# Kernel optimization log

Measured on AMD Instinct MI355X. Metric: run time of the kernel, lower is better.

Reference implementation:

```python
import jax, jax.numpy as jnp
import numpy as np
import math

B, C, T = 4, 512, 2048
H = 8            # num_heads
G = 32           # GroupNorm groups (GroupNorm32 in ADM-style code)
EPS = 1e-5


def setup_inputs() -> dict:
    key = jax.random.key(0)
    ks = jax.random.split(key, 7)
    x = jax.random.normal(ks[0], (B, C, T), jnp.float32)
    norm_scale = 1.0 + 0.02 * jax.random.normal(ks[1], (C,), jnp.float32)
    norm_bias = 0.02 * jax.random.normal(ks[2], (C,), jnp.float32)
    qkv_w = 0.02 * jax.random.normal(ks[3], (3 * C, C), jnp.float32)  # 1x1 conv == matmul
    qkv_b = 0.02 * jax.random.normal(ks[4], (3 * C,), jnp.float32)
    proj_w = 0.02 * jax.random.normal(ks[5], (C, C), jnp.float32)
    proj_b = 0.02 * jax.random.normal(ks[6], (C,), jnp.float32)
    return {"x": x, "norm_scale": norm_scale, "norm_bias": norm_bias,
            "qkv_w": qkv_w, "qkv_b": qkv_b, "proj_w": proj_w, "proj_b": proj_b}


def _group_norm(x, scale, bias):
    # x: [B, C, T]; 32-group norm over (C/G, T) per group
    b, c, t = x.shape
    xg = x.reshape(b, G, (c // G) * t)
    mean = jnp.mean(xg, axis=-1, keepdims=True)
    var = jnp.var(xg, axis=-1, keepdims=True)
    xg = (xg - mean) * jax.lax.rsqrt(var + EPS)
    return xg.reshape(b, c, t) * scale[None, :, None] + bias[None, :, None]


def reference(x, norm_scale, norm_bias, qkv_w, qkv_b, proj_w, proj_b):
    b, c, t = x.shape
    ch = c // H
    h = _group_norm(x, norm_scale, norm_bias)
    qkv = jnp.einsum('oc,bct->bot', qkv_w, h) + qkv_b[None, :, None]  # [B, 3C, T]
    q, k, v = jnp.split(qkv, 3, axis=1)
    q = q.reshape(b * H, ch, t)
    k = k.reshape(b * H, ch, t)
    v = v.reshape(b * H, ch, t)
    scale = 1.0 / math.sqrt(math.sqrt(ch))
    w = jnp.einsum('bct,bcs->bts', q * scale, k * scale)              # [B*H, T, T]
    w = jax.nn.softmax(w.astype(jnp.float32), axis=-1).astype(qkv.dtype)
    a = jnp.einsum('bts,bcs->bct', w, v).reshape(b, c, t)             # [B, C, T]
    out = jnp.einsum('oc,bct->bot', proj_w, a) + proj_b[None, :, None]
    return x + out
```

## Files before the change

kernel.cpp:

```cpp
#include <hip/hip_runtime.h>

typedef short bf16x8 __attribute__((ext_vector_type(8)));
typedef float f32x4 __attribute__((ext_vector_type(4)));
typedef float f32x16 __attribute__((ext_vector_type(16)));
typedef unsigned short u16;
typedef unsigned int u32;

constexpr int B = 4, C = 512, T = 2048, H = 8, G = 32;
constexpr int CH = C / H;
constexpr int CPG = C / G;
constexpr float EPS = 1e-5f;
constexpr float SCLQ = 0.18033688011112042f;

__device__ __forceinline__ u16 f2bf(float f) {
  union { float f; u32 u; } v; v.f = f;
  return (u16)((v.u + 0x7FFFu + ((v.u >> 16) & 1u)) >> 16);
}

__device__ __forceinline__ u32 cvtpk(float lo, float hi) {
  u32 r;
  asm("v_cvt_pk_bf16_f32 %0, %1, %2" : "=v"(r) : "v"(lo), "v"(hi));
  return r;
}

__device__ __forceinline__ void gload16(const void* g, void* lds) {
  __builtin_amdgcn_global_load_lds(
      (const __attribute__((address_space(1))) void*)g,
      (__attribute__((address_space(3))) void*)lds, 16, 0, 0);
}

__device__ __forceinline__ void pl32swap(u32& a, u32& b) {
  asm("v_permlane32_swap_b32 %0, %1" : "+v"(a), "+v"(b));
}

template <int ROWS>
__device__ __forceinline__ void stage_swz_8w(u16* lds, const u16* gsrc, int ldk) {
  const int tid = threadIdx.x;
  const int w = tid >> 6, lane = tid & 63;
#pragma unroll
  for (int i = 0; i < ROWS / 64; ++i) {
    const int chunk = i * 8 + w;
    const int row = chunk * 8 + (lane >> 3);
    const int col = ((lane & 7) * 8) ^ ((row & 7) << 3);
    gload16(gsrc + (size_t)row * ldk + col, (char*)lds + chunk * 1024);
  }
}

__global__ __launch_bounds__(256) void prep_k(const float* __restrict__ x,
                                              float* __restrict__ stats,
                                              const float* __restrict__ s1,
                                              u16* __restrict__ d1, int n1,
                                              const float* __restrict__ s2,
                                              u16* __restrict__ d2, int n2) {
  __shared__ float red[8];
  const int bid = blockIdx.x;
  if (bid >= 128) {
    int i = (bid - 128) * 256 + threadIdx.x;
    const float4* src = (const float4*)s1;
    uint2* dst = (uint2*)d1;
    if (i >= n1) { i -= n1; if (i >= n2) return; src = (const float4*)s2; dst = (uint2*)d2; }
    float4 v = src[i];
    uint2 pk;
    pk.x = cvtpk(v.x, v.y);
    pk.y = cvtpk(v.z, v.w);
    dst[i] = pk;
    return;
  }
  const int bg = bid;
  const float4* xp = (const float4*)(x + (size_t)bg * CPG * T);
  float s = 0.f, ss = 0.f;
  for (int i = threadIdx.x; i < CPG * T / 4; i += 256) {
    float4 v = xp[i];
    s += v.x + v.y + v.z + v.w;
    ss += v.x * v.x + v.y * v.y + v.z * v.z + v.w * v.w;
  }
  for (int off = 32; off; off >>= 1) {
    s += __shfl_down(s, off);
    ss += __shfl_down(ss, off);
  }
  const int w = threadIdx.x >> 6;
  if ((threadIdx.x & 63) == 0) { red[w] = s; red[4 + w] = ss; }
  __syncthreads();
  if (threadIdx.x == 0) {
    float S = red[0] + red[1] + red[2] + red[3];
    float SS = red[4] + red[5] + red[6] + red[7];
    const float inv = 1.f / (float)(CPG * T);
    float mean = S * inv;
    float var = SS * inv - mean * mean;
    stats[bg * 2] = mean;
    stats[bg * 2 + 1] = rsqrtf(var + EPS);
  }
}

__global__ __launch_bounds__(256) void gn_apply_k(const float* __restrict__ x,
                                                  const float* __restrict__ stats,
                                                  const float* __restrict__ gsc,
                                                  const float* __restrict__ gbi,
                                                  u16* __restrict__ ht) {
  const int b = blockIdx.y;
  const int t0 = blockIdx.x * 16;
#pragma unroll
  for (int p = 0; p < 2; ++p) {
    const int c = p * 256 + threadIdx.x;
    const int bg = b * G + (c >> 4);
    const float mean = stats[bg * 2], rstd = stats[bg * 2 + 1];
    const float sc = gsc[c] * rstd;
    const float bi = gbi[c] - mean * sc;
    const float4* xp = (const float4*)(x + ((size_t)b * C + c) * T + t0);
#pragma unroll
    for (int j = 0; j < 4; ++j) {
      float4 v = xp[j];
      const int t = t0 + j * 4;
      u16* hp = ht + ((size_t)b * T + t) * C + c;
      hp[0]     = f2bf(v.x * sc + bi);
      hp[C]     = f2bf(v.y * sc + bi);
      hp[2 * C] = f2bf(v.z * sc + bi);
      hp[3 * C] = f2bf(v.w * sc + bi);
    }
  }
}

__global__ __launch_bounds__(512, 2) void qkv_gemm_k(const u16* __restrict__ ht,
                                                     const u16* __restrict__ wq,
                                                     const float* __restrict__ qkvb,
                                                     u16* __restrict__ qo,
                                                     u16* __restrict__ kvo_k,
                                                     u16* __restrict__ kvo_v) {
  __shared__ u16 As[2][128 * 64];
  __shared__ u16 Bs[2][128 * 64];
  const int bid = blockIdx.x;
  const int wg = (bid & 7) * 96 + (bid >> 3);
  const int nt = wg % 12;
  const int mtb = wg / 12;
  const int mt = mtb & 15, b = mtb >> 4;
  const u16* Ab = ht + ((size_t)b * T + mt * 128) * C;
  const u16* Bb = wq + (size_t)nt * 128 * C;
  const int tid = threadIdx.x, lane = tid & 63, w = tid >> 6;
  const int wr = w >> 1, wc = w & 1, l15 = lane & 15, lhi = lane >> 4;
  const int swz = (l15 & 7) << 3;
  constexpr int NK = C / 64;

  const f32x4 vzero = {0.f, 0.f, 0.f, 0.f};
  f32x4 acc[2][4];
#pragma unroll
  for (int m = 0; m < 2; ++m)
#pragma unroll
    for (int n = 0; n < 4; ++n) acc[m][n] = vzero;

  stage_swz_8w<128>(As[0], Ab, C);
  stage_swz_8w<128>(Bs[0], Bb, C);
  asm volatile("s_waitcnt vmcnt(0)" ::: "memory");
  __builtin_amdgcn_s_barrier();
  asm volatile("" ::: "memory");

  int cur = 0;
  for (int kt = 0; kt < NK; ++kt) {
    if (kt + 1 < NK) {
      stage_swz_8w<128>(As[cur ^ 1], Ab + (kt + 1) * 64, C);
      stage_swz_8w<128>(Bs[cur ^ 1], Bb + (kt + 1) * 64, C);
    }
#pragma unroll
    for (int kk = 0; kk < 2; ++kk) {
      const int koff = (kk * 32 + lhi * 8) ^ swz;
      bf16x8 af[2], bfv[4];
#pragma unroll
      for (int m = 0; m < 2; ++m)
        af[m] = *(const bf16x8*)&As[cur][(wr * 32 + m * 16 + l15) * 64 + koff];
#pragma unroll
      for (int n = 0; n < 4; ++n)
        bfv[n] = *(const bf16x8*)&Bs[cur][(wc * 64 + n * 16 + l15) * 64 + koff];
#pragma unroll
      for (int m = 0; m < 2; ++m)
#pragma unroll
        for (int n = 0; n < 4; ++n)
          acc[m][n] = __builtin_amdgcn_mfma_f32_16x16x32_bf16(af[m], bfv[n], acc[m][n], 0, 0, 0);
    }
    if (kt + 1 < NK) {
      asm volatile("s_waitcnt vmcnt(0)" ::: "memory");
      __builtin_amdgcn_s_barrier();
      asm volatile("" ::: "memory");
    }
    cur ^= 1;
  }
#pragma unroll
  for (int n = 0; n < 4; ++n) {
    const int o = nt * 128 + wc * 64 + n * 16 + l15;
    const float bias = qkvb[o];
    const int which = o >> 9, rem = o & 511, hh = rem >> 6, d = rem & 63;
    const size_t bh = (size_t)b * H + hh;
#pragma unroll
    for (int m = 0; m < 2; ++m) {
      const int tbase = mt * 128 + wr * 32 + m * 16 + lhi * 4;
      float v0 = acc[m][n][0] + bias, v1 = acc[m][n][1] + bias;
      float v2 = acc[m][n][2] + bias, v3 = acc[m][n][3] + bias;
      if (which == 0) { v0 *= SCLQ; v1 *= SCLQ; v2 *= SCLQ; v3 *= SCLQ; }
      const u32 w01 = cvtpk(v0, v1), w23 = cvtpk(v2, v3);
      if (which == 2) {
        uint2 pk; pk.x = w01; pk.y = w23;
        *(uint2*)&kvo_v[(bh * CH + d) * T + tbase] = pk;
      } else {
        u16* dst = (which == 0) ? qo : kvo_k;
        dst[(bh * T + tbase) * CH + d]     = (u16)(w01 & 0xffff);
        dst[(bh * T + tbase + 1) * CH + d] = (u16)(w01 >> 16);
        dst[(bh * T + tbase + 2) * CH + d] = (u16)(w23 & 0xffff);
        dst[(bh * T + tbase + 3) * CH + d] = (u16)(w23 >> 16);
      }
    }
  }
}

__global__ __launch_bounds__(512, 4) void attn_k(const u16* __restrict__ q,
                                                 const u16* __restrict__ k,
                                                 const u16* __restrict__ v,
                                                 u16* __restrict__ at) {
  __shared__ u16 Ks[2][128 * 64];
  __shared__ u16 Vs[2][2][64 * 64];
  const int lin = blockIdx.x + (blockIdx.y << 4);
  const int wg = (lin & 7) * 64 + (lin >> 3);
  const int qt = wg & 15, bh = wg >> 4;
  const int tid = threadIdx.x, lane = tid & 63, w = tid >> 6;
  const int qset = w & 3, grp = w >> 2;
  const int l31 = lane & 31, h = lane >> 5;
  const u16* qb = q + (size_t)bh * T * CH;
  const u16* kb = k + (size_t)bh * T * CH;
  const u16* vb = v + (size_t)bh * CH * T;
  constexpr int NP = T / 128;

  bf16x8 qf[4];
  {
    const u16* qp = qb + (size_t)(qt * 128 + qset * 32 + l31) * CH + h * 8;
#pragma unroll
    for (int ks = 0; ks < 4; ++ks) qf[ks] = *(const bf16x8*)(qp + ks * 16);
  }
  union { u32 u[4]; bf16x8 v8; } ones;
#pragma unroll
  for (int i = 0; i < 4; ++i) ones.u[i] = 0x3F803F80u;

  stage_swz_8w<128>(Ks[0], kb, CH);
  stage_swz_8w<64>(Vs[0][0], vb, T);
  stage_swz_8w<64>(Vs[0][1], vb + 64, T);
  asm volatile("s_waitcnt vmcnt(0)" ::: "memory");
  __builtin_amdgcn_s_barrier();
  asm volatile("" ::: "memory");

  f32x16 accO0 = {0.f,0.f,0.f,0.f,0.f,0.f,0.f,0.f,0.f,0.f,0.f,0.f,0.f,0.f,0.f,0.f};
  f32x16 accO1 = accO0;
  f32x16 accL = accO0;
  const int kswz = (l31 & 7) << 3;

  int cur = 0;
  for (int p = 0; p < NP; ++p) {
    if (p + 1 < NP) {
      stage_swz_8w<128>(Ks[cur ^ 1], kb + (size_t)(p + 1) * 128 * CH, CH);
      stage_swz_8w<64>(Vs[cur ^ 1][0], vb + (p + 1) * 128, T);
      stage_swz_8w<64>(Vs[cur ^ 1][1], vb + (p + 1) * 128 + 64, T);
    }
    const u16* Kc = &Ks[cur][grp * 64 * 64];
    const u16* Vc = Vs[cur][grp];

    f32x16 accS0 = {0.f,0.f,0.f,0.f,0.f,0.f,0.f,0.f,0.f,0.f,0.f,0.f,0.f,0.f,0.f,0.f};
    f32x16 accS1 = accS0;
    __builtin_amdgcn_s_setprio(1);
#pragma unroll
    for (int ks = 0; ks < 4; ++ks) {
      const int col = (ks * 16 + h * 8) ^ kswz;
      bf16x8 kf0 = *(const bf16x8*)&Kc[l31 * 64 + col];
      bf16x8 kf1 = *(const bf16x8*)&Kc[(32 + l31) * 64 + col];
      accS0 = __builtin_amdgcn_mfma_f32_32x32x16_bf16(kf0, qf[ks], accS0, 0, 0, 0);
      accS1 = __builtin_amdgcn_mfma_f32_32x32x16_bf16(kf1, qf[ks], accS1, 0, 0, 0);
    }
    __builtin_amdgcn_s_setprio(0);

    u32 wd0[8], wd1[8];
#pragma unroll
    for (int i = 0; i < 8; ++i) {
      float pa = __builtin_amdgcn_exp2f(accS0[2 * i]);
      float pb = __builtin_amdgcn_exp2f(accS0[2 * i + 1]);
      asm("v_cvt_pk_bf16_f32 %0, %1, %2" : "=v"(wd0[i]) : "v"(pa), "v"(pb));
    }
#pragma unroll
    for (int i = 0; i < 8; ++i) {
      float pa = __builtin_amdgcn_exp2f(accS1[2 * i]);
      float pb = __builtin_amdgcn_exp2f(accS1[2 * i + 1]);
      asm("v_cvt_pk_bf16_f32 %0, %1, %2" : "=v"(wd1[i]) : "v"(pa), "v"(pb));
    }
    pl32swap(wd0[0], wd0[2]); pl32swap(wd0[1], wd0[3]);
    pl32swap(wd0[4], wd0[6]); pl32swap(wd0[5], wd0[7]);
    pl32swap(wd1[0], wd1[2]); pl32swap(wd1[1], wd1[3]);
    pl32swap(wd1[4], wd1[6]); pl32swap(wd1[5], wd1[7]);

    __builtin_amdgcn_s_setprio(1);
#pragma unroll
    for (int kt = 0; kt < 2; ++kt) {
      const u32* wd = kt ? wd1 : wd0;
      union { u32 u[4]; bf16x8 v8; } fa, fb;
      fa.u[0] = wd[0]; fa.u[1] = wd[1]; fa.u[2] = wd[2]; fa.u[3] = wd[3];
      fb.u[0] = wd[4]; fb.u[1] = wd[5]; fb.u[2] = wd[6]; fb.u[3] = wd[7];
      const int sA = (kt * 32 + h * 8) ^ kswz;
      const int sB = (kt * 32 + 16 + h * 8) ^ kswz;
      {
        bf16x8 vf0 = *(const bf16x8*)&Vc[l31 * 64 + sA];
        bf16x8 vf1 = *(const bf16x8*)&Vc[l31 * 64 + sB];
        accO0 = __builtin_amdgcn_mfma_f32_32x32x16_bf16(fa.v8, vf0, accO0, 0, 0, 0);
        accO0 = __builtin_amdgcn_mfma_f32_32x32x16_bf16(fb.v8, vf1, accO0, 0, 0, 0);
      }
      {
        bf16x8 vf0 = *(const bf16x8*)&Vc[(32 + l31) * 64 + sA];
        bf16x8 vf1 = *(const bf16x8*)&Vc[(32 + l31) * 64 + sB];
        accO1 = __builtin_amdgcn_mfma_f32_32x32x16_bf16(fa.v8, vf0, accO1, 0, 0, 0);
        accO1 = __builtin_amdgcn_mfma_f32_32x32x16_bf16(fb.v8, vf1, accO1, 0, 0, 0);
      }
      accL = __builtin_amdgcn_mfma_f32_32x32x16_bf16(fa.v8, ones.v8, accL, 0, 0, 0);
      accL = __builtin_amdgcn_mfma_f32_32x32x16_bf16(fb.v8, ones.v8, accL, 0, 0, 0);
    }
    __builtin_amdgcn_s_setprio(0);

    asm volatile("s_waitcnt vmcnt(0)" ::: "memory");
    __builtin_amdgcn_s_barrier();
    asm volatile("" ::: "memory");
    cur ^= 1;
  }

  float* fO = (float*)&Ks[0][0];
  float* fL = (float*)&Vs[0][0][0];
  if (grp == 1) {
#pragma unroll
    for (int r = 0; r < 16; ++r) {
      const int qrow = (r & 3) + 8 * (r >> 2) + 4 * h;
      float* row = fO + (qset * 32 + qrow) * 64;
      row[l31] = accO0[r];
      row[32 + l31] = accO1[r];
      if (l31 == 0) fL[qset * 32 + qrow] = accL[r];
    }
  }
  __syncthreads();
  if (grp == 0) {
    const int bq = bh >> 3, hh = bh & 7;
#pragma unroll
    for (int r = 0; r < 16; ++r) {
      const int qrow = (r & 3) + 8 * (r >> 2) + 4 * h;
      const float denom = accL[r] + fL[qset * 32 + qrow];
      const float invr = __builtin_amdgcn_rcpf(denom);
      const float* row = fO + (qset * 32 + qrow) * 64;
      const float o0 = accO0[r] + row[l31];
      const float o1 = accO1[r] + row[32 + l31];
      const int t = qt * 128 + qset * 32 + qrow;
      u16* op = at + ((size_t)bq * T + t) * C + hh * 64 + l31;
      op[0]  = f2bf(o0 * invr);
      op[32] = f2bf(o1 * invr);
    }
  }
}

__global__ __launch_bounds__(512, 2) void proj_gemm_k(const u16* __restrict__ at,
                                                      const u16* __restrict__ wp,
                                                      const float* __restrict__ pb,
                                                      const float* __restrict__ x,
                                                      float* __restrict__ out) {
  __shared__ u16 As[2][128 * 64];
  __shared__ u16 Bs[2][64 * 64];
  const int bid = blockIdx.x;
  const int wg = (bid & 7) * 64 + (bid >> 3);
  const int nt = wg & 7;
  const int mtb = wg >> 3;
  const int mt = mtb & 15, b = mtb >> 4;
  const u16* Ab = at + ((size_t)b * T + mt * 128) * C;
  const u16* Bb = wp + (size_t)nt * 64 * C;
  const int tid = threadIdx.x, lane = tid & 63, w = tid >> 6;
  const int l15 = lane & 15, lhi = lane >> 4;
  const int swz = (l15 & 7) << 3;
  constexpr int NK = C / 64;

  const f32x4 vzero = {0.f, 0.f, 0.f, 0.f};
  f32x4 acc[4];
#pragma unroll
  for (int n = 0; n < 4; ++n) acc[n] = vzero;

  stage_swz_8w<128>(As[0], Ab, C);
  stage_swz_8w<64>(Bs[0], Bb, C);
  asm volatile("s_waitcnt vmcnt(0)" ::: "memory");
  __builtin_amdgcn_s_barrier();
  asm volatile("" ::: "memory");

  int cur = 0;
  for (int kt = 0; kt < NK; ++kt) {
    if (kt + 1 < NK) {
      stage_swz_8w<128>(As[cur ^ 1], Ab + (kt + 1) * 64, C);
      stage_swz_8w<64>(Bs[cur ^ 1], Bb + (kt + 1) * 64, C);
    }
#pragma unroll
    for (int kk = 0; kk < 2; ++kk) {
      const int koff = (kk * 32 + lhi * 8) ^ swz;
      bf16x8 af = *(const bf16x8*)&As[cur][(w * 16 + l15) * 64 + koff];
      bf16x8 bfv[4];
#pragma unroll
      for (int n = 0; n < 4; ++n)
        bfv[n] = *(const bf16x8*)&Bs[cur][(n * 16 + l15) * 64 + koff];
#pragma unroll
      for (int n = 0; n < 4; ++n)
        acc[n] = __builtin_amdgcn_mfma_f32_16x16x32_bf16(af, bfv[n], acc[n], 0, 0, 0);
    }
    if (kt + 1 < NK) {
      asm volatile("s_waitcnt vmcnt(0)" ::: "memory");
      __builtin_amdgcn_s_barrier();
      asm volatile("" ::: "memory");
    }
    cur ^= 1;
  }
#pragma unroll
  for (int n = 0; n < 4; ++n) {
    const int o = nt * 64 + n * 16 + l15;
    const float bias = pb[o];
    const int tbase = mt * 128 + w * 16 + lhi * 4;
    const size_t idx = ((size_t)b * C + o) * T + tbase;
    const float4 xv = *(const float4*)&x[idx];
    float4 ov;
    ov.x = xv.x + acc[n][0] + bias;
    ov.y = xv.y + acc[n][1] + bias;
    ov.z = xv.z + acc[n][2] + bias;
    ov.w = xv.w + acc[n][3] + bias;
    *(float4*)&out[idx] = ov;
  }
}

extern "C" void kernel_launch(void* const* d_in, const int* in_sizes, int n_in,
                              void* d_out, int out_size, void* d_ws, size_t ws_size,
                              hipStream_t stream) {
  const float* x     = (const float*)d_in[0];
  const float* gsc   = (const float*)d_in[1];
  const float* gbi   = (const float*)d_in[2];
  const float* qkvw  = (const float*)d_in[3];
  const float* qkvb  = (const float*)d_in[4];
  const float* projw = (const float*)d_in[5];
  const float* projb = (const float*)d_in[6];
  float* out = (float*)d_out;

  char* ws = (char*)d_ws;
  float* stats = (float*)ws;
  u16* wq = (u16*)(ws + 1024);
  u16* wp = (u16*)(ws + 1024 + 1572864);
  u16* ht = (u16*)(ws + 2098176);
  u16* qo = (u16*)(ws + 10486784);
  u16* ko = (u16*)(ws + 18875392);
  u16* vo = (u16*)(ws + 27264000);
  u16* at = ht;

  prep_k<<<1152, 256, 0, stream>>>(x, stats, qkvw, wq, 196608, projw, wp, 65536);
  gn_apply_k<<<dim3(T / 16, B), 256, 0, stream>>>(x, stats, gsc, gbi, ht);
  qkv_gemm_k<<<768, 512, 0, stream>>>(ht, wq, qkvb, qo, ko, vo);
  attn_k<<<dim3(T / 128, B * H), 512, 0, stream>>>(qo, ko, vo, at);
  proj_gemm_k<<<512, 512, 0, stream>>>(at, wp, projb, x, out);
}
```

Before: 104.4 us.

## Fuse GroupNorm apply into QKV GEMM A-tile staging

Removes the separate gn_apply kernel. The QKV GEMM now loads fp32 x directly, applies the GroupNorm scale and bias in registers, converts to bf16 and writes the swizzled A tile into LDS itself. This drops one launch and the write and re-read of the bf16 normalized activation buffer. In exchange each GEMM block reads fp32 x (twice the bytes, and once per N tile, so 12 times), does scattered 2-byte LDS stores, and occupancy hint is raised to 4 blocks.

```diff
diff --git a/kernel.cpp b/kernel.cpp
--- a/kernel.cpp
+++ b/kernel.cpp
@@ -44,6 +44,10 @@
     const int col = ((lane & 7) * 8) ^ ((row & 7) << 3);
     gload16(gsrc + (size_t)row * ldk + col, (char*)lds + chunk * 1024);
   }
+}
+
+__device__ __forceinline__ int a_idx(int t, int c) {
+  return t * 64 + ((((c >> 3) ^ (t & 7)) << 3) | (c & 7));
 }
 
 __global__ __launch_bounds__(256) void prep_k(const float* __restrict__ x,
@@ -92,35 +96,10 @@
   }
 }
 
-__global__ __launch_bounds__(256) void gn_apply_k(const float* __restrict__ x,
-                                                  const float* __restrict__ stats,
-                                                  const float* __restrict__ gsc,
-                                                  const float* __restrict__ gbi,
-                                                  u16* __restrict__ ht) {
-  const int b = blockIdx.y;
-  const int t0 = blockIdx.x * 16;
-#pragma unroll
-  for (int p = 0; p < 2; ++p) {
-    const int c = p * 256 + threadIdx.x;
-    const int bg = b * G + (c >> 4);
-    const float mean = stats[bg * 2], rstd = stats[bg * 2 + 1];
-    const float sc = gsc[c] * rstd;
-    const float bi = gbi[c] - mean * sc;
-    const float4* xp = (const float4*)(x + ((size_t)b * C + c) * T + t0);
-#pragma unroll
-    for (int j = 0; j < 4; ++j) {
-      float4 v = xp[j];
-      const int t = t0 + j * 4;
-      u16* hp = ht + ((size_t)b * T + t) * C + c;
-      hp[0]     = f2bf(v.x * sc + bi);
-      hp[C]     = f2bf(v.y * sc + bi);
-      hp[2 * C] = f2bf(v.z * sc + bi);
-      hp[3 * C] = f2bf(v.w * sc + bi);
-    }
-  }
-}
-
-__global__ __launch_bounds__(512, 2) void qkv_gemm_k(const u16* __restrict__ ht,
+__global__ __launch_bounds__(512, 4) void qkv_gemm_k(const float* __restrict__ x,
+                                                     const float* __restrict__ stats,
+                                                     const float* __restrict__ gsc,
+                                                     const float* __restrict__ gbi,
                                                      const u16* __restrict__ wq,
                                                      const float* __restrict__ qkvb,
                                                      u16* __restrict__ qo,
@@ -133,13 +112,16 @@
   const int nt = wg % 12;
   const int mtb = wg / 12;
   const int mt = mtb & 15, b = mtb >> 4;
-  const u16* Ab = ht + ((size_t)b * T + mt * 128) * C;
   const u16* Bb = wq + (size_t)nt * 128 * C;
   const int tid = threadIdx.x, lane = tid & 63, w = tid >> 6;
   const int wr = w >> 1, wc = w & 1, l15 = lane & 15, lhi = lane >> 4;
   const int swz = (l15 & 7) << 3;
   constexpr int NK = C / 64;
 
+  const float* xcol0 = x + ((size_t)b * C + lane) * T + mt * 128 + w * 16;
+  float4 xs[4];
+  float n_sc, n_bi;
+
   const f32x4 vzero = {0.f, 0.f, 0.f, 0.f};
   f32x4 acc[2][4];
 #pragma unroll
@@ -147,16 +129,40 @@
 #pragma unroll
     for (int n = 0; n < 4; ++n) acc[m][n] = vzero;
 
-  stage_swz_8w<128>(As[0], Ab, C);
+  {
+    const float4* xp = (const float4*)xcol0;
+#pragma unroll
+    for (int j = 0; j < 4; ++j) xs[j] = xp[j];
+    const int bg = b * G + (lane >> 4);
+    const float mean = stats[bg * 2], rstd = stats[bg * 2 + 1];
+    n_sc = gsc[lane] * rstd;
+    n_bi = gbi[lane] - mean * n_sc;
+  }
   stage_swz_8w<128>(Bs[0], Bb, C);
   asm volatile("s_waitcnt vmcnt(0)" ::: "memory");
-  __builtin_amdgcn_s_barrier();
-  asm volatile("" ::: "memory");
+#pragma unroll
+  for (int j = 0; j < 4; ++j) {
+    const int t = w * 16 + j * 4;
+    const u32 p01 = cvtpk(xs[j].x * n_sc + n_bi, xs[j].y * n_sc + n_bi);
+    const u32 p23 = cvtpk(xs[j].z * n_sc + n_bi, xs[j].w * n_sc + n_bi);
+    As[0][a_idx(t, lane)]     = (u16)p01;
+    As[0][a_idx(t + 1, lane)] = (u16)(p01 >> 16);
+    As[0][a_idx(t + 2, lane)] = (u16)p23;
+    As[0][a_idx(t + 3, lane)] = (u16)(p23 >> 16);
+  }
+  __syncthreads();
 
   int cur = 0;
   for (int kt = 0; kt < NK; ++kt) {
     if (kt + 1 < NK) {
-      stage_swz_8w<128>(As[cur ^ 1], Ab + (kt + 1) * 64, C);
+      const int c1 = (kt + 1) * 64 + lane;
+      const float4* xp = (const float4*)(xcol0 + (size_t)(kt + 1) * 64 * T);
+#pragma unroll
+      for (int j = 0; j < 4; ++j) xs[j] = xp[j];
+      const int bg = b * G + (c1 >> 4);
+      const float mean = stats[bg * 2], rstd = stats[bg * 2 + 1];
+      n_sc = gsc[c1] * rstd;
+      n_bi = gbi[c1] - mean * n_sc;
       stage_swz_8w<128>(Bs[cur ^ 1], Bb + (kt + 1) * 64, C);
     }
 #pragma unroll
@@ -177,8 +183,18 @@
     }
     if (kt + 1 < NK) {
       asm volatile("s_waitcnt vmcnt(0)" ::: "memory");
-      __builtin_amdgcn_s_barrier();
-      asm volatile("" ::: "memory");
+      u16* dst = As[cur ^ 1];
+#pragma unroll
+      for (int j = 0; j < 4; ++j) {
+        const int t = w * 16 + j * 4;
+        const u32 p01 = cvtpk(xs[j].x * n_sc + n_bi, xs[j].y * n_sc + n_bi);
+        const u32 p23 = cvtpk(xs[j].z * n_sc + n_bi, xs[j].w * n_sc + n_bi);
+        dst[a_idx(t, lane)]     = (u16)p01;
+        dst[a_idx(t + 1, lane)] = (u16)(p01 >> 16);
+        dst[a_idx(t + 2, lane)] = (u16)p23;
+        dst[a_idx(t + 3, lane)] = (u16)(p23 >> 16);
+      }
+      __syncthreads();
     }
     cur ^= 1;
   }
@@ -439,15 +455,13 @@
   float* stats = (float*)ws;
   u16* wq = (u16*)(ws + 1024);
   u16* wp = (u16*)(ws + 1024 + 1572864);
-  u16* ht = (u16*)(ws + 2098176);
+  u16* at = (u16*)(ws + 2098176);
   u16* qo = (u16*)(ws + 10486784);
   u16* ko = (u16*)(ws + 18875392);
   u16* vo = (u16*)(ws + 27264000);
-  u16* at = ht;
 
   prep_k<<<1152, 256, 0, stream>>>(x, stats, qkvw, wq, 196608, projw, wp, 65536);
-  gn_apply_k<<<dim3(T / 16, B), 256, 0, stream>>>(x, stats, gsc, gbi, ht);
-  qkv_gemm_k<<<768, 512, 0, stream>>>(ht, wq, qkvb, qo, ko, vo);
+  qkv_gemm_k<<<768, 512, 0, stream>>>(x, stats, gsc, gbi, wq, qkvb, qo, ko, vo);
   attn_k<<<dim3(T / 128, B * H), 512, 0, stream>>>(qo, ko, vo, at);
   proj_gemm_k<<<512, 512, 0, stream>>>(at, wp, projb, x, out);
 }
```

After: 113.0 us. +8.2%, slower.
